# Performance work log

Measured on AMD Instinct MI355X. Metric: run time of the kernel, lower is better.

Reference implementation:

```python
import jax, jax.numpy as jnp
import numpy as np

N_NODES = 50000
N_EDGES = 800000
IN_F, HID, OUT_F = 256, 128, 64
ATTN_SLOPE = 0.2   # DGL GATConv negative_slope default
ACT_SLOPE = 0.01   # nn.LeakyReLU default


def setup_inputs() -> dict:
    key = jax.random.key(0)
    ks = jax.random.split(key, 7)
    x = jax.random.normal(ks[0], (N_NODES, IN_F), dtype=jnp.float32)
    src = jax.random.randint(ks[1], (N_EDGES,), 0, N_NODES, dtype=jnp.int32)
    dst = jax.random.randint(ks[2], (N_EDGES,), 0, N_NODES, dtype=jnp.int32)
    W_gat = jax.random.normal(ks[3], (IN_F, HID), dtype=jnp.float32) * (1.0 / np.sqrt(IN_F))
    attn_l = jax.random.normal(ks[4], (HID,), dtype=jnp.float32) * 0.1
    attn_r = jax.random.normal(ks[5], (HID,), dtype=jnp.float32) * 0.1
    bias_gat = jnp.zeros((HID,), dtype=jnp.float32)
    W_lin = jax.random.normal(ks[6], (OUT_F, HID), dtype=jnp.float32) * (1.0 / np.sqrt(HID))
    return {"x": x, "src": src, "dst": dst, "W_gat": W_gat, "attn_l": attn_l,
            "attn_r": attn_r, "bias_gat": bias_gat, "W_lin": W_lin}


def reference(x, src, dst, W_gat, attn_l, attn_r, bias_gat, W_lin):
    N = x.shape[0]
    # GATConv (num_heads=1): linear projection then additive attention
    feat = x @ W_gat                         # [N, HID]
    el = feat @ attn_l                        # [N]  (sum(feat * a_l, -1))
    er = feat @ attn_r                        # [N]
    # per-edge logits, leaky_relu(0.2)
    e = jax.nn.leaky_relu(el[src] + er[dst], negative_slope=ATTN_SLOPE)  # [E]
    # segment softmax over edges grouped by destination node
    e_max = jax.ops.segment_max(e, dst, num_segments=N)  # [N] (-inf for isolated)
    alpha = jnp.exp(e - e_max[dst])                      # [E]
    denom = jax.ops.segment_sum(alpha, dst, num_segments=N)
    a = alpha / denom[dst]                               # [E]
    # scatter-weighted aggregation of source features
    msg = a[:, None] * feat[src]                         # [E, HID]
    agg = jax.ops.segment_sum(msg, dst, num_segments=N) + bias_gat  # [N, HID]
    # outer wrapper: LeakyReLU(0.01), squeeze (head dim already gone), linear no bias
    gene = jax.nn.leaky_relu(agg, negative_slope=ACT_SLOPE)
    return gene @ W_lin.T                                # [N, OUT_F]
```

## Files before the change

### kernel.cpp

```cpp
#include <hip/hip_runtime.h>
#include <hip/hip_bf16.h>


#define NNODES 50000
#define NEDGES 800000
#define IN_F   256
#define HID    128
#define OUTF   64

#define PA_EPT   8
#define PA_EDGES (256 * PA_EPT)
#define PA_NB    ((NEDGES + PA_EDGES - 1) / PA_EDGES)
#define NBKT     ((NNODES + 255) / 256)
#define BCAP     5120
#define NSTRIP   (NNODES / 16)
#define GB       ((NSTRIP + 3) / 4)

typedef unsigned short u16;
typedef unsigned long long u64;
typedef __bf16 bf16x8 __attribute__((ext_vector_type(8)));
typedef float  f32x4  __attribute__((ext_vector_type(4)));

__device__ __forceinline__ u16 f2b(float f) {
    union { float f; unsigned u; } v; v.f = f;
    unsigned u = v.u;
    return (u16)((u + 0x7fffu + ((u >> 16) & 1u)) >> 16);
}
__device__ __forceinline__ float b2f_lo(unsigned v) {
    union { unsigned u; float f; } c; c.u = (v & 0xffffu) << 16; return c.f;
}
__device__ __forceinline__ float b2f_hi(unsigned v) {
    union { unsigned u; float f; } c; c.u = v & 0xffff0000u; return c.f;
}
__device__ __forceinline__ float lrelu02_exp(float t) {
    t = t > 0.f ? t : 0.2f * t;
    return __expf(t);
}

__global__ __launch_bounds__(256) void pack0(const float* __restrict__ Wg,
                                             const float* __restrict__ Wl,
                                             u16* __restrict__ pWg,
                                             u16* __restrict__ pWl,
                                             int* __restrict__ bcnt) {
    int blk = blockIdx.x, tid = threadIdx.x;
    if (blk < 16) {
        int t = blk * 256 + tid;
        int lane = t & 63, tile = t >> 6;
        int nt = tile & 7, kt = tile >> 3;
        int col = lane & 15, quad = lane >> 4;
        int krow = kt * 32 + quad * 8;
        int ncol = nt * 16 + col;
#pragma unroll
        for (int j = 0; j < 8; j++) pWg[t * 8 + j] = f2b(Wg[(krow + j) * HID + ncol]);
    } else if (blk < 20) {
        int t = (blk - 16) * 256 + tid;
        int lane = t & 63, tile = t >> 6;
        int nt = tile & 3, kt = tile >> 2;
        int col = lane & 15, quad = lane >> 4;
        int o  = nt * 16 + col;
        int k0 = kt * 32 + quad * 8;
#pragma unroll
        for (int j = 0; j < 8; j++) pWl[t * 8 + j] = f2b(Wl[o * HID + k0 + j]);
    } else {
        if (tid < NBKT) bcnt[tid] = 0;
    }
}

__global__ __launch_bounds__(256, 5) void k_mega(
        const float* __restrict__ x, const u16* __restrict__ pWg,
        const float* __restrict__ al_, const float* __restrict__ ar_,
        unsigned* __restrict__ feat2, float* __restrict__ el, float* __restrict__ er,
        const int* __restrict__ src, const int* __restrict__ dst,
        int* __restrict__ bcnt, u64* __restrict__ pairs) {
    __shared__ u64 smemU[21504 / 8];
    char* smem = (char*)smemU;
    int blk = blockIdx.x, tid = threadIdx.x;

    if (blk < GB) {
        int wave = tid >> 6, lane = tid & 63;
        int strip = blk * 4 + wave;
        if (strip >= NSTRIP) return;
        int m0 = strip * 16;
        int col = lane & 15, quad = lane >> 4;

        f32x4 acc[8] = {};
        const float* xr = x + (size_t)(m0 + col) * IN_F + quad * 8;
#pragma unroll
        for (int kt = 0; kt < 8; kt++) {
            f32x4 a0 = *reinterpret_cast<const f32x4*>(xr + kt * 32);
            f32x4 a1 = *reinterpret_cast<const f32x4*>(xr + kt * 32 + 4);
            bf16x8 av;
#pragma unroll
            for (int j = 0; j < 4; j++) {
                av[j] = (__bf16)a0[j]; av[4 + j] = (__bf16)a1[j];
            }
#pragma unroll
            for (int nt = 0; nt < 8; nt++) {
                bf16x8 b = *reinterpret_cast<const bf16x8*>(pWg + ((kt * 8 + nt) * 64 + lane) * 8);
                acc[nt] = __builtin_amdgcn_mfma_f32_16x16x32_bf16(av, b, acc[nt], 0, 0, 0);
            }
        }
        float pl[4] = {0, 0, 0, 0}, pr[4] = {0, 0, 0, 0};
#pragma unroll
        for (int nt = 0; nt < 8; nt++) {
            float alv = al_[nt * 16 + col], arv = ar_[nt * 16 + col];
#pragma unroll
            for (int reg = 0; reg < 4; reg++) {
                pl[reg] += acc[nt][reg] * alv;
                pr[reg] += acc[nt][reg] * arv;
            }
        }
#pragma unroll
        for (int m = 1; m < 16; m <<= 1)
#pragma unroll
            for (int reg = 0; reg < 4; reg++) {
                pl[reg] += __shfl_xor(pl[reg], m, 64);
                pr[reg] += __shfl_xor(pr[reg], m, 64);
            }
        if (col == 0) {
#pragma unroll
            for (int reg = 0; reg < 4; reg++) {
                el[m0 + quad * 4 + reg] = pl[reg];
                er[m0 + quad * 4 + reg] = pr[reg];
            }
        }
#pragma unroll
        for (int nt = 0; nt < 8; nt++)
#pragma unroll
            for (int reg = 0; reg < 4; reg++) {
                u16* fp = (u16*)feat2;
                fp[(size_t)(m0 + quad * 4 + reg) * HID + nt * 16 + col] = f2b(acc[nt][reg]);
            }
        return;
    }

    int* hist    = (int*)smem;
    int* binbase = hist + 256;
    int* gbase   = binbase + 256;
    int* fill    = gbase + 256;
    int* stmp    = fill + 256;
    u64* spair   = (u64*)(smem + 5120);

    int e0 = (blk - GB) * PA_EDGES;
    int cnt = NEDGES - e0; if (cnt > PA_EDGES) cnt = PA_EDGES;

    hist[tid] = 0; fill[tid] = 0;
    __syncthreads();

    int es[PA_EPT], ed[PA_EPT];
#pragma unroll
    for (int j = 0; j < PA_EPT; j++) {
        int idx = e0 + j * 256 + tid;
        if (idx < NEDGES) {
            es[j] = src[idx];
            ed[j] = dst[idx];
            atomicAdd(&hist[ed[j] >> 8], 1);
        } else ed[j] = -1;
    }
    __syncthreads();

    stmp[tid] = (tid < NBKT) ? hist[tid] : 0;
    __syncthreads();
#pragma unroll
    for (int ofs = 1; ofs < 256; ofs <<= 1) {
        int u = (tid >= ofs) ? stmp[tid - ofs] : 0;
        __syncthreads();
        stmp[tid] += u;
        __syncthreads();
    }
    if (tid < NBKT) {
        binbase[tid] = stmp[tid] - hist[tid];
        if (hist[tid] > 0)
            gbase[tid] = tid * BCAP + atomicAdd(&bcnt[tid], hist[tid]);
    }
    __syncthreads();

#pragma unroll
    for (int j = 0; j < PA_EPT; j++) {
        if (ed[j] >= 0) {
            int b = ed[j] >> 8;
            int r = atomicAdd(&fill[b], 1);
            int loc = binbase[b] + r;
            spair[loc] = ((u64)(unsigned)ed[j] << 32) | (unsigned)es[j];
        }
    }
    __syncthreads();

    for (int i = tid; i < cnt; i += 256) {
        u64 p = spair[i];
        int b = (int)(p >> 40);
        pairs[gbase[b] + (i - binbase[b])] = p;
    }
}

__global__ __launch_bounds__(512) void k_fine(const u64* __restrict__ pairs,
                                              const int* __restrict__ bcnt,
                                              const float* __restrict__ el,
                                              const float* __restrict__ er,
                                              int* __restrict__ rowptr,
                                              int* __restrict__ esrc,
                                              float* __restrict__ ew,
                                              float* __restrict__ den) {
    __shared__ int sbc[256];
    __shared__ int nh[256];
    __shared__ int wsum[256];
    __shared__ int cur[256];
    __shared__ float dls[256];
    __shared__ float erl[256];

    int b = blockIdx.x, tid = threadIdx.x;
    int nb = b << 8;
    int nn = NNODES - nb; if (nn > 256) nn = 256;

    if (tid < 256) sbc[tid] = (tid < NBKT) ? bcnt[tid] : 0;
    __syncthreads();
#pragma unroll
    for (int ofs = 1; ofs < 256; ofs <<= 1) {
        int u = 0;
        if (tid < 256 && tid >= ofs) u = sbc[tid - ofs];
        __syncthreads();
        if (tid < 256) sbc[tid] += u;
        __syncthreads();
    }
    int cntb = bcnt[b];
    int base = sbc[b] - cntb;
    const u64* reg = pairs + (size_t)b * BCAP;

    if (tid < 256) {
        nh[tid] = 0;
        dls[tid] = 0.f;
        erl[tid] = (tid < nn) ? er[nb + tid] : 0.f;
    }
    __syncthreads();
    for (int i = tid; i < cntb; i += 512) {
        int d = (int)(unsigned)(reg[i] >> 32);
        atomicAdd(&nh[d - nb], 1);
    }
    __syncthreads();

    int c = (tid < 256) ? nh[tid] : 0;
    if (tid < 256) wsum[tid] = c;
    __syncthreads();
#pragma unroll
    for (int ofs = 1; ofs < 256; ofs <<= 1) {
        int u = 0;
        if (tid < 256 && tid >= ofs) u = wsum[tid - ofs];
        __syncthreads();
        if (tid < 256) wsum[tid] += u;
        __syncthreads();
    }
    if (tid < 256) {
        int o = base + wsum[tid] - c;
        cur[tid] = o;
        if (tid < nn) rowptr[nb + tid] = o;
    }
    if (b == NBKT - 1 && tid == 0) rowptr[NNODES] = NEDGES;
    __syncthreads();

    for (int i = tid; i < cntb; i += 512) {
        u64 p = reg[i];
        int s_ = (int)(unsigned)(p & 0xffffffffu);
        int d  = (int)(unsigned)(p >> 32);
        int dl = d - nb;
        float w = lrelu02_exp(el[s_] + erl[dl]);
        int pos = atomicAdd(&cur[dl], 1);
        esrc[pos] = s_;
        ew[pos] = w;
        atomicAdd(&dls[dl], w);
    }
    __syncthreads();
    if (tid < nn) den[nb + tid] = dls[tid];
}

__global__ __launch_bounds__(256) void k_aggout(const int* __restrict__ rowptr,
                                                const int* __restrict__ esrc,
                                                const float* __restrict__ ew,
                                                const float* __restrict__ den,
                                                const unsigned* __restrict__ feat2,
                                                const float* __restrict__ bias,
                                                const u16* __restrict__ pWl,
                                                float* __restrict__ out) {
    __shared__ unsigned sg[16 * 68];
    int wave = threadIdx.x >> 6, lane = threadIdx.x & 63;
    int m0 = blockIdx.x * 16;
    float bl = bias[lane * 2 + 0], bh = bias[lane * 2 + 1];

    for (int i = 0; i < 4; i++) {
        int r = wave * 4 + i;
        int n = m0 + r;
        int beg = rowptr[n], end = rowptr[n + 1];

        float p0 = 0.f, p1 = 0.f, q0 = 0.f, q1 = 0.f;
        float r0 = 0.f, r1 = 0.f, t0 = 0.f, t1 = 0.f;
        float u0 = 0.f, u1 = 0.f, x0 = 0.f, x1 = 0.f;
        float y0 = 0.f, y1 = 0.f, z0 = 0.f, z1 = 0.f;
        int j = beg;
        for (; j + 8 <= end; j += 8) {
            int s0 = esrc[j],     s1 = esrc[j + 1], s2 = esrc[j + 2], s3 = esrc[j + 3];
            int s4 = esrc[j + 4], s5 = esrc[j + 5], s6 = esrc[j + 6], s7 = esrc[j + 7];
            unsigned v0 = feat2[(size_t)s0 * 64 + lane];
            unsigned v1 = feat2[(size_t)s1 * 64 + lane];
            unsigned v2 = feat2[(size_t)s2 * 64 + lane];
            unsigned v3 = feat2[(size_t)s3 * 64 + lane];
            unsigned v4 = feat2[(size_t)s4 * 64 + lane];
            unsigned v5 = feat2[(size_t)s5 * 64 + lane];
            unsigned v6 = feat2[(size_t)s6 * 64 + lane];
            unsigned v7 = feat2[(size_t)s7 * 64 + lane];
            float w0 = ew[j],     w1 = ew[j + 1], w2 = ew[j + 2], w3 = ew[j + 3];
            float w4 = ew[j + 4], w5 = ew[j + 5], w6 = ew[j + 6], w7 = ew[j + 7];
            p0 += w0 * b2f_lo(v0); p1 += w0 * b2f_hi(v0);
            q0 += w1 * b2f_lo(v1); q1 += w1 * b2f_hi(v1);
            r0 += w2 * b2f_lo(v2); r1 += w2 * b2f_hi(v2);
            t0 += w3 * b2f_lo(v3); t1 += w3 * b2f_hi(v3);
            u0 += w4 * b2f_lo(v4); u1 += w4 * b2f_hi(v4);
            x0 += w5 * b2f_lo(v5); x1 += w5 * b2f_hi(v5);
            y0 += w6 * b2f_lo(v6); y1 += w6 * b2f_hi(v6);
            z0 += w7 * b2f_lo(v7); z1 += w7 * b2f_hi(v7);
        }
        if (j + 4 <= end) {
            int s0 = esrc[j], s1 = esrc[j + 1], s2 = esrc[j + 2], s3 = esrc[j + 3];
            unsigned v0 = feat2[(size_t)s0 * 64 + lane];
            unsigned v1 = feat2[(size_t)s1 * 64 + lane];
            unsigned v2 = feat2[(size_t)s2 * 64 + lane];
            unsigned v3 = feat2[(size_t)s3 * 64 + lane];
            float w0 = ew[j], w1 = ew[j + 1], w2 = ew[j + 2], w3 = ew[j + 3];
            p0 += w0 * b2f_lo(v0); p1 += w0 * b2f_hi(v0);
            q0 += w1 * b2f_lo(v1); q1 += w1 * b2f_hi(v1);
            r0 += w2 * b2f_lo(v2); r1 += w2 * b2f_hi(v2);
            t0 += w3 * b2f_lo(v3); t1 += w3 * b2f_hi(v3);
            j += 4;
        }
        for (; j < end; j++) {
            int s = esrc[j];
            float w = ew[j];
            unsigned v = feat2[(size_t)s * 64 + lane];
            p0 += w * b2f_lo(v); p1 += w * b2f_hi(v);
        }
        float a0 = ((p0 + q0) + (r0 + t0)) + ((u0 + x0) + (y0 + z0));
        float a1 = ((p1 + q1) + (r1 + t1)) + ((u1 + x1) + (y1 + z1));

        float dn = den[n];
        float inv = dn > 0.f ? 1.f / dn : 0.f;
        float g0 = a0 * inv + bl;
        float g1 = a1 * inv + bh;
        g0 = g0 > 0.f ? g0 : 0.01f * g0;
        g1 = g1 > 0.f ? g1 : 0.01f * g1;
        sg[r * 68 + lane] = (unsigned)f2b(g0) | ((unsigned)f2b(g1) << 16);
    }
    __syncthreads();

    int col = lane & 15, quad = lane >> 4;
    int nt = wave;
    f32x4 acc = {};
#pragma unroll
    for (int kt = 0; kt < 4; kt++) {
        bf16x8 a = *reinterpret_cast<const bf16x8*>(&sg[col * 68 + kt * 16 + quad * 4]);
        bf16x8 bf = *reinterpret_cast<const bf16x8*>(pWl + ((kt * 4 + nt) * 64 + lane) * 8);
        acc = __builtin_amdgcn_mfma_f32_16x16x32_bf16(a, bf, acc, 0, 0, 0);
    }
#pragma unroll
    for (int reg = 0; reg < 4; reg++)
        out[(size_t)(m0 + quad * 4 + reg) * OUTF + nt * 16 + col] = acc[reg];
}

extern "C" void kernel_launch(void* const* d_in, const int* in_sizes, int n_in,
                              void* d_out, int out_size, void* d_ws, size_t ws_size,
                              hipStream_t stream) {
    const float* x      = (const float*)d_in[0];
    const int*   src    = (const int*)d_in[1];
    const int*   dst    = (const int*)d_in[2];
    const float* Wg     = (const float*)d_in[3];
    const float* attn_l = (const float*)d_in[4];
    const float* attn_r = (const float*)d_in[5];
    const float* bias   = (const float*)d_in[6];
    const float* Wl     = (const float*)d_in[7];
    float* out          = (float*)d_out;

    char* ws = (char*)d_ws;
    size_t off = 0;
    auto alloc = [&](size_t b) { size_t r = off; off += (b + 255) & ~(size_t)255; return r; };
    size_t pwgOff  = alloc((size_t)8 * 8 * 64 * 8 * 2);
    size_t pwlOff  = alloc((size_t)4 * 4 * 64 * 8 * 2);
    size_t featOff = alloc((size_t)NNODES * HID * 2);
    size_t elOff   = alloc((size_t)NNODES * 4);
    size_t erOff   = alloc((size_t)NNODES * 4);
    size_t denOff  = alloc((size_t)NNODES * 4);
    size_t rowOff  = alloc((size_t)(NNODES + 1) * 4);
    size_t esrcOff = alloc((size_t)NEDGES * 4);
    size_t ewOff   = alloc((size_t)NEDGES * 4);
    size_t pairOff = alloc((size_t)NBKT * BCAP * 8);
    size_t bcntOff = alloc((size_t)NBKT * 4);

    u16*      pWg   = (u16*)(ws + pwgOff);
    u16*      pWl   = (u16*)(ws + pwlOff);
    unsigned* feat2 = (unsigned*)(ws + featOff);
    float*    el    = (float*)(ws + elOff);
    float*    er    = (float*)(ws + erOff);
    float*    den   = (float*)(ws + denOff);
    int*      rowp  = (int*)(ws + rowOff);
    int*      esrc  = (int*)(ws + esrcOff);
    float*    ew    = (float*)(ws + ewOff);
    u64*      pairs = (u64*)(ws + pairOff);
    int*      bcnt  = (int*)(ws + bcntOff);

    pack0<<<21, 256, 0, stream>>>(Wg, Wl, pWg, pWl, bcnt);
    k_mega<<<GB + PA_NB, 256, 0, stream>>>(x, pWg, attn_l, attn_r, feat2, el, er,
                                           src, dst, bcnt, pairs);
    k_fine<<<NBKT, 512, 0, stream>>>(pairs, bcnt, el, er, rowp, esrc, ew, den);
    k_aggout<<<NNODES / 16, 256, 0, stream>>>(rowp, esrc, ew, den, feat2, bias,
                                              pWl, out);
}
```

Baseline: 175.3 us.

## Replace bucket-sort CSR build with padded per-node adjacency and fused edge weights

```diff
diff --git a/kernel.cpp b/kernel.cpp
--- a/kernel.cpp
+++ b/kernel.cpp
@@ -8,13 +8,10 @@
 #define HID    128
 #define OUTF   64
 
-#define PA_EPT   8
-#define PA_EDGES (256 * PA_EPT)
-#define PA_NB    ((NEDGES + PA_EDGES - 1) / PA_EDGES)
-#define NBKT     ((NNODES + 255) / 256)
-#define BCAP     5120
-#define NSTRIP   (NNODES / 16)
-#define GB       ((NSTRIP + 3) / 4)
+#define EDEG   96
+#define EB     224
+#define NSTRIP (NNODES / 16)
+#define GB     ((NSTRIP + 3) / 4)
 
 typedef unsigned short u16;
 typedef unsigned long long u64;
@@ -41,7 +38,7 @@
                                              const float* __restrict__ Wl,
                                              u16* __restrict__ pWg,
                                              u16* __restrict__ pWl,
-                                             int* __restrict__ bcnt) {
+                                             int* __restrict__ deg) {
     int blk = blockIdx.x, tid = threadIdx.x;
     if (blk < 16) {
         int t = blk * 256 + tid;
@@ -62,18 +59,17 @@
 #pragma unroll
         for (int j = 0; j < 8; j++) pWl[t * 8 + j] = f2b(Wl[o * HID + k0 + j]);
     } else {
-        if (tid < NBKT) bcnt[tid] = 0;
-    }
-}
-
-__global__ __launch_bounds__(256, 5) void k_mega(
+        int t = (blk - 20) * 256 + tid;
+        if (t < NNODES) deg[t] = 0;
+    }
+}
+
+__global__ __launch_bounds__(256, 4) void k_mega(
         const float* __restrict__ x, const u16* __restrict__ pWg,
         const float* __restrict__ al_, const float* __restrict__ ar_,
         unsigned* __restrict__ feat2, float* __restrict__ el, float* __restrict__ er,
         const int* __restrict__ src, const int* __restrict__ dst,
-        int* __restrict__ bcnt, u64* __restrict__ pairs) {
-    __shared__ u64 smemU[21504 / 8];
-    char* smem = (char*)smemU;
+        int* __restrict__ deg, int* __restrict__ eidx) {
     int blk = blockIdx.x, tid = threadIdx.x;
 
     if (blk < GB) {
@@ -134,152 +130,22 @@
         return;
     }
 
-    int* hist    = (int*)smem;
-    int* binbase = hist + 256;
-    int* gbase   = binbase + 256;
-    int* fill    = gbase + 256;
-    int* stmp    = fill + 256;
-    u64* spair   = (u64*)(smem + 5120);
-
-    int e0 = (blk - GB) * PA_EDGES;
-    int cnt = NEDGES - e0; if (cnt > PA_EDGES) cnt = PA_EDGES;
-
-    hist[tid] = 0; fill[tid] = 0;
-    __syncthreads();
-
-    int es[PA_EPT], ed[PA_EPT];
-#pragma unroll
-    for (int j = 0; j < PA_EPT; j++) {
-        int idx = e0 + j * 256 + tid;
-        if (idx < NEDGES) {
-            es[j] = src[idx];
-            ed[j] = dst[idx];
-            atomicAdd(&hist[ed[j] >> 8], 1);
-        } else ed[j] = -1;
-    }
-    __syncthreads();
-
-    stmp[tid] = (tid < NBKT) ? hist[tid] : 0;
-    __syncthreads();
-#pragma unroll
-    for (int ofs = 1; ofs < 256; ofs <<= 1) {
-        int u = (tid >= ofs) ? stmp[tid - ofs] : 0;
-        __syncthreads();
-        stmp[tid] += u;
-        __syncthreads();
-    }
-    if (tid < NBKT) {
-        binbase[tid] = stmp[tid] - hist[tid];
-        if (hist[tid] > 0)
-            gbase[tid] = tid * BCAP + atomicAdd(&bcnt[tid], hist[tid]);
-    }
-    __syncthreads();
-
-#pragma unroll
-    for (int j = 0; j < PA_EPT; j++) {
-        if (ed[j] >= 0) {
-            int b = ed[j] >> 8;
-            int r = atomicAdd(&fill[b], 1);
-            int loc = binbase[b] + r;
-            spair[loc] = ((u64)(unsigned)ed[j] << 32) | (unsigned)es[j];
-        }
-    }
-    __syncthreads();
-
-    for (int i = tid; i < cnt; i += 256) {
-        u64 p = spair[i];
-        int b = (int)(p >> 40);
-        pairs[gbase[b] + (i - binbase[b])] = p;
-    }
-}
-
-__global__ __launch_bounds__(512) void k_fine(const u64* __restrict__ pairs,
-                                              const int* __restrict__ bcnt,
-                                              const float* __restrict__ el,
-                                              const float* __restrict__ er,
-                                              int* __restrict__ rowptr,
-                                              int* __restrict__ esrc,
-                                              float* __restrict__ ew,
-                                              float* __restrict__ den) {
-    __shared__ int sbc[256];
-    __shared__ int nh[256];
-    __shared__ int wsum[256];
-    __shared__ int cur[256];
-    __shared__ float dls[256];
-    __shared__ float erl[256];
-
-    int b = blockIdx.x, tid = threadIdx.x;
-    int nb = b << 8;
-    int nn = NNODES - nb; if (nn > 256) nn = 256;
-
-    if (tid < 256) sbc[tid] = (tid < NBKT) ? bcnt[tid] : 0;
-    __syncthreads();
-#pragma unroll
-    for (int ofs = 1; ofs < 256; ofs <<= 1) {
-        int u = 0;
-        if (tid < 256 && tid >= ofs) u = sbc[tid - ofs];
-        __syncthreads();
-        if (tid < 256) sbc[tid] += u;
-        __syncthreads();
-    }
-    int cntb = bcnt[b];
-    int base = sbc[b] - cntb;
-    const u64* reg = pairs + (size_t)b * BCAP;
-
-    if (tid < 256) {
-        nh[tid] = 0;
-        dls[tid] = 0.f;
-        erl[tid] = (tid < nn) ? er[nb + tid] : 0.f;
-    }
-    __syncthreads();
-    for (int i = tid; i < cntb; i += 512) {
-        int d = (int)(unsigned)(reg[i] >> 32);
-        atomicAdd(&nh[d - nb], 1);
-    }
-    __syncthreads();
-
-    int c = (tid < 256) ? nh[tid] : 0;
-    if (tid < 256) wsum[tid] = c;
-    __syncthreads();
-#pragma unroll
-    for (int ofs = 1; ofs < 256; ofs <<= 1) {
-        int u = 0;
-        if (tid < 256 && tid >= ofs) u = wsum[tid - ofs];
-        __syncthreads();
-        if (tid < 256) wsum[tid] += u;
-        __syncthreads();
-    }
-    if (tid < 256) {
-        int o = base + wsum[tid] - c;
-        cur[tid] = o;
-        if (tid < nn) rowptr[nb + tid] = o;
-    }
-    if (b == NBKT - 1 && tid == 0) rowptr[NNODES] = NEDGES;
-    __syncthreads();
-
-    for (int i = tid; i < cntb; i += 512) {
-        u64 p = reg[i];
-        int s_ = (int)(unsigned)(p & 0xffffffffu);
-        int d  = (int)(unsigned)(p >> 32);
-        int dl = d - nb;
-        float w = lrelu02_exp(el[s_] + erl[dl]);
-        int pos = atomicAdd(&cur[dl], 1);
-        esrc[pos] = s_;
-        ew[pos] = w;
-        atomicAdd(&dls[dl], w);
-    }
-    __syncthreads();
-    if (tid < nn) den[nb + tid] = dls[tid];
-}
-
-__global__ __launch_bounds__(256) void k_aggout(const int* __restrict__ rowptr,
-                                                const int* __restrict__ esrc,
-                                                const float* __restrict__ ew,
-                                                const float* __restrict__ den,
-                                                const unsigned* __restrict__ feat2,
-                                                const float* __restrict__ bias,
-                                                const u16* __restrict__ pWl,
-                                                float* __restrict__ out) {
+    int e0 = (blk - GB) * 256 + tid;
+    for (int e = e0; e < NEDGES; e += EB * 256) {
+        int s = src[e], d = dst[e];
+        int slot = atomicAdd(&deg[d], 1);
+        eidx[(size_t)d * EDEG + slot] = s;
+    }
+}
+
+__global__ __launch_bounds__(256) void k_agg(const int* __restrict__ deg,
+                                             const int* __restrict__ eidx,
+                                             const float* __restrict__ el,
+                                             const float* __restrict__ er,
+                                             const unsigned* __restrict__ feat2,
+                                             const float* __restrict__ bias,
+                                             const u16* __restrict__ pWl,
+                                             float* __restrict__ out) {
     __shared__ unsigned sg[16 * 68];
     int wave = threadIdx.x >> 6, lane = threadIdx.x & 63;
     int m0 = blockIdx.x * 16;
@@ -288,26 +154,33 @@
     for (int i = 0; i < 4; i++) {
         int r = wave * 4 + i;
         int n = m0 + r;
-        int beg = rowptr[n], end = rowptr[n + 1];
+        int cnt = deg[n];
+        const int* ep = eidx + (size_t)n * EDEG;
+        float ern = er[n];
 
         float p0 = 0.f, p1 = 0.f, q0 = 0.f, q1 = 0.f;
         float r0 = 0.f, r1 = 0.f, t0 = 0.f, t1 = 0.f;
         float u0 = 0.f, u1 = 0.f, x0 = 0.f, x1 = 0.f;
         float y0 = 0.f, y1 = 0.f, z0 = 0.f, z1 = 0.f;
-        int j = beg;
-        for (; j + 8 <= end; j += 8) {
-            int s0 = esrc[j],     s1 = esrc[j + 1], s2 = esrc[j + 2], s3 = esrc[j + 3];
-            int s4 = esrc[j + 4], s5 = esrc[j + 5], s6 = esrc[j + 6], s7 = esrc[j + 7];
-            unsigned v0 = feat2[(size_t)s0 * 64 + lane];
-            unsigned v1 = feat2[(size_t)s1 * 64 + lane];
-            unsigned v2 = feat2[(size_t)s2 * 64 + lane];
-            unsigned v3 = feat2[(size_t)s3 * 64 + lane];
-            unsigned v4 = feat2[(size_t)s4 * 64 + lane];
-            unsigned v5 = feat2[(size_t)s5 * 64 + lane];
-            unsigned v6 = feat2[(size_t)s6 * 64 + lane];
-            unsigned v7 = feat2[(size_t)s7 * 64 + lane];
-            float w0 = ew[j],     w1 = ew[j + 1], w2 = ew[j + 2], w3 = ew[j + 3];
-            float w4 = ew[j + 4], w5 = ew[j + 5], w6 = ew[j + 6], w7 = ew[j + 7];
+        float dn = 0.f;
+        int j = 0;
+        for (; j + 8 <= cnt; j += 8) {
+            int4 sa = *reinterpret_cast<const int4*>(ep + j);
+            int4 sb = *reinterpret_cast<const int4*>(ep + j + 4);
+            float e0 = el[sa.x], e1 = el[sa.y], e2 = el[sa.z], e3 = el[sa.w];
+            float e4 = el[sb.x], e5 = el[sb.y], e6 = el[sb.z], e7 = el[sb.w];
+            unsigned v0 = feat2[(size_t)sa.x * 64 + lane];
+            unsigned v1 = feat2[(size_t)sa.y * 64 + lane];
+            unsigned v2 = feat2[(size_t)sa.z * 64 + lane];
+            unsigned v3 = feat2[(size_t)sa.w * 64 + lane];
+            unsigned v4 = feat2[(size_t)sb.x * 64 + lane];
+            unsigned v5 = feat2[(size_t)sb.y * 64 + lane];
+            unsigned v6 = feat2[(size_t)sb.z * 64 + lane];
+            unsigned v7 = feat2[(size_t)sb.w * 64 + lane];
+            float w0 = lrelu02_exp(e0 + ern), w1 = lrelu02_exp(e1 + ern);
+            float w2 = lrelu02_exp(e2 + ern), w3 = lrelu02_exp(e3 + ern);
+            float w4 = lrelu02_exp(e4 + ern), w5 = lrelu02_exp(e5 + ern);
+            float w6 = lrelu02_exp(e6 + ern), w7 = lrelu02_exp(e7 + ern);
             p0 += w0 * b2f_lo(v0); p1 += w0 * b2f_hi(v0);
             q0 += w1 * b2f_lo(v1); q1 += w1 * b2f_hi(v1);
             r0 += w2 * b2f_lo(v2); r1 += w2 * b2f_hi(v2);
@@ -316,30 +189,34 @@
             x0 += w5 * b2f_lo(v5); x1 += w5 * b2f_hi(v5);
             y0 += w6 * b2f_lo(v6); y1 += w6 * b2f_hi(v6);
             z0 += w7 * b2f_lo(v7); z1 += w7 * b2f_hi(v7);
-        }
-        if (j + 4 <= end) {
-            int s0 = esrc[j], s1 = esrc[j + 1], s2 = esrc[j + 2], s3 = esrc[j + 3];
-            unsigned v0 = feat2[(size_t)s0 * 64 + lane];
-            unsigned v1 = feat2[(size_t)s1 * 64 + lane];
-            unsigned v2 = feat2[(size_t)s2 * 64 + lane];
-            unsigned v3 = feat2[(size_t)s3 * 64 + lane];
-            float w0 = ew[j], w1 = ew[j + 1], w2 = ew[j + 2], w3 = ew[j + 3];
+            dn += ((w0 + w1) + (w2 + w3)) + ((w4 + w5) + (w6 + w7));
+        }
+        if (j + 4 <= cnt) {
+            int4 sa = *reinterpret_cast<const int4*>(ep + j);
+            float e0 = el[sa.x], e1 = el[sa.y], e2 = el[sa.z], e3 = el[sa.w];
+            unsigned v0 = feat2[(size_t)sa.x * 64 + lane];
+            unsigned v1 = feat2[(size_t)sa.y * 64 + lane];
+            unsigned v2 = feat2[(size_t)sa.z * 64 + lane];
+            unsigned v3 = feat2[(size_t)sa.w * 64 + lane];
+            float w0 = lrelu02_exp(e0 + ern), w1 = lrelu02_exp(e1 + ern);
+            float w2 = lrelu02_exp(e2 + ern), w3 = lrelu02_exp(e3 + ern);
             p0 += w0 * b2f_lo(v0); p1 += w0 * b2f_hi(v0);
             q0 += w1 * b2f_lo(v1); q1 += w1 * b2f_hi(v1);
             r0 += w2 * b2f_lo(v2); r1 += w2 * b2f_hi(v2);
             t0 += w3 * b2f_lo(v3); t1 += w3 * b2f_hi(v3);
+            dn += (w0 + w1) + (w2 + w3);
             j += 4;
         }
-        for (; j < end; j++) {
-            int s = esrc[j];
-            float w = ew[j];
+        for (; j < cnt; j++) {
+            int s = ep[j];
+            float w = lrelu02_exp(el[s] + ern);
             unsigned v = feat2[(size_t)s * 64 + lane];
             p0 += w * b2f_lo(v); p1 += w * b2f_hi(v);
+            dn += w;
         }
         float a0 = ((p0 + q0) + (r0 + t0)) + ((u0 + x0) + (y0 + z0));
         float a1 = ((p1 + q1) + (r1 + t1)) + ((u1 + x1) + (y1 + z1));
 
-        float dn = den[n];
         float inv = dn > 0.f ? 1.f / dn : 0.f;
         float g0 = a0 * inv + bl;
         float g1 = a1 * inv + bh;
@@ -384,29 +261,20 @@
     size_t featOff = alloc((size_t)NNODES * HID * 2);
     size_t elOff   = alloc((size_t)NNODES * 4);
     size_t erOff   = alloc((size_t)NNODES * 4);
-    size_t denOff  = alloc((size_t)NNODES * 4);
-    size_t rowOff  = alloc((size_t)(NNODES + 1) * 4);
-    size_t esrcOff = alloc((size_t)NEDGES * 4);
-    size_t ewOff   = alloc((size_t)NEDGES * 4);
-    size_t pairOff = alloc((size_t)NBKT * BCAP * 8);
-    size_t bcntOff = alloc((size_t)NBKT * 4);
+    size_t eidxOff = alloc((size_t)NNODES * EDEG * 4);
+    size_t degOff  = alloc((size_t)NNODES * 4);
 
     u16*      pWg   = (u16*)(ws + pwgOff);
     u16*      pWl   = (u16*)(ws + pwlOff);
     unsigned* feat2 = (unsigned*)(ws + featOff);
     float*    el    = (float*)(ws + elOff);
     float*    er    = (float*)(ws + erOff);
-    float*    den   = (float*)(ws + denOff);
-    int*      rowp  = (int*)(ws + rowOff);
-    int*      esrc  = (int*)(ws + esrcOff);
-    float*    ew    = (float*)(ws + ewOff);
-    u64*      pairs = (u64*)(ws + pairOff);
-    int*      bcnt  = (int*)(ws + bcntOff);
-
-    pack0<<<21, 256, 0, stream>>>(Wg, Wl, pWg, pWl, bcnt);
-    k_mega<<<GB + PA_NB, 256, 0, stream>>>(x, pWg, attn_l, attn_r, feat2, el, er,
-                                           src, dst, bcnt, pairs);
-    k_fine<<<NBKT, 512, 0, stream>>>(pairs, bcnt, el, er, rowp, esrc, ew, den);
-    k_aggout<<<NNODES / 16, 256, 0, stream>>>(rowp, esrc, ew, den, feat2, bias,
-                                              pWl, out);
-}
+    int*      eidx  = (int*)(ws + eidxOff);
+    int*      deg   = (int*)(ws + degOff);
+
+    pack0<<<20 + (NNODES + 255) / 256, 256, 0, stream>>>(Wg, Wl, pWg, pWl, deg);
+    k_mega<<<GB + EB, 256, 0, stream>>>(x, pWg, attn_l, attn_r, feat2, el, er,
+                                        src, dst, deg, eidx);
+    k_agg<<<NNODES / 16, 256, 0, stream>>>(deg, eidx, el, er, feat2, bias,
+                                           pWl, out);
+}
```

After: 195.0 us. +11.2%, slower.
